# Optimization experiments

Measured on AMD Instinct MI355X. Metric: run time of the kernel, lower is better.

## Reference

```python
import jax, jax.numpy as jnp
import numpy as np

NUM_HEADS = 16


def setup_inputs() -> dict:
    key = jax.random.key(0)
    ks = jax.random.split(key, 6)
    B, T, C = 2, 1024, 2048
    H, D = NUM_HEADS, C // NUM_HEADS
    Tc = 1024  # cached tokens
    return {
        "x": jax.random.normal(ks[0], (B, T, C), dtype=jnp.float32),
        "cache_k": jax.random.normal(ks[1], (B, H, Tc, D), dtype=jnp.float32),
        "cache_v": jax.random.normal(ks[2], (B, H, Tc, D), dtype=jnp.float32),
        "W_qkv": jax.random.normal(ks[3], (C, 3 * C), dtype=jnp.float32) * (C ** -0.5),
        "W_proj": jax.random.normal(ks[4], (C, C), dtype=jnp.float32) * (C ** -0.5),
        "b_proj": jnp.zeros((C,), dtype=jnp.float32),
        "seq_start": Tc,
    }


def reference(x, cache_k, cache_v, W_qkv, W_proj, b_proj, seq_start):
    B, T, C = x.shape
    H = NUM_HEADS
    D = C // H
    scale = D ** -0.5

    qkv = (x @ W_qkv).reshape(B, T, 3, H, D)
    # (B, H, T, D)
    q = jnp.transpose(qkv[:, :, 0], (0, 2, 1, 3))
    k = jnp.transpose(qkv[:, :, 1], (0, 2, 1, 3))
    v = jnp.transpose(qkv[:, :, 2], (0, 2, 1, 3))

    # append to KV cache along time axis
    k = jnp.concatenate([cache_k, k], axis=2)
    v = jnp.concatenate([cache_v, v], axis=2)
    k_len = k.shape[2]

    # causal mask on absolute positions: query_pos >= key_pos
    query_pos = seq_start + jnp.arange(T)
    key_pos = jnp.arange(k_len)
    causal = query_pos[:, None] >= key_pos[None, :]  # (T, k_len)

    attn = jnp.einsum("bhqd,bhkd->bhqk", q * scale, k)
    attn = jnp.where(causal[None, None], attn, -jnp.inf)
    attn = jax.nn.softmax(attn, axis=-1)

    out = jnp.einsum("bhqk,bhkd->bhqd", attn, v)
    out = jnp.transpose(out, (0, 2, 1, 3)).reshape(B, T, C)
    out = out @ W_proj + b_proj
    return out, k, v
```

## Files before the change

### kernel.cpp

```cpp
#include <hip/hip_runtime.h>
#include <hip/hip_bf16.h>

typedef __attribute__((ext_vector_type(8))) short bf16x8;
typedef __attribute__((ext_vector_type(4))) float f32x4;
typedef __attribute__((ext_vector_type(16))) float f32x16;

#define DI __device__ __forceinline__

static constexpr int Bb  = 2;
static constexpr int Tt  = 1024;
static constexpr int Cc  = 2048;
static constexpr int Hh  = 16;
static constexpr int Dd  = 128;
static constexpr int TC  = 1024;
static constexpr int CTX = 2048;
static constexpr float QSCALE = 0.08838834764831845f;

DI unsigned short f2bf(float f){
  unsigned u = __builtin_bit_cast(unsigned, f);
  u += 0x7FFFu + ((u >> 16) & 1u);
  return (unsigned short)(u >> 16);
}
DI float bf2f(unsigned short s){
  return __builtin_bit_cast(float, (unsigned)s << 16);
}
DI unsigned pk2(float a, float b){
  return (unsigned)f2bf(a) | ((unsigned)f2bf(b) << 16);
}
DI bf16x8 mk4(unsigned a, unsigned b, unsigned c, unsigned d){
  union{ unsigned u[4]; bf16x8 v; } x;
  x.u[0]=a; x.u[1]=b; x.u[2]=c; x.u[3]=d; return x.v;
}
DI f32x16 mfma32(bf16x8 a, bf16x8 b, f32x16 c){
  return __builtin_amdgcn_mfma_f32_32x32x16_bf16(a, b, c, 0, 0, 0);
}
#define MFMA16(a,b,c) __builtin_amdgcn_mfma_f32_16x16x32_bf16(a,b,c,0,0,0)
DI void gld16(const void* g, void* l){
  __builtin_amdgcn_global_load_lds(
      (const __attribute__((address_space(1))) unsigned int*)g,
      (__attribute__((address_space(3))) unsigned int*)l, 16, 0, 0);
}
DI unsigned ldsoff(const void* p){
  return (unsigned)(size_t)(const __attribute__((address_space(3))) void*)p;
}
template<int OFF>
DI bf16x8 dsr(unsigned addr){
  bf16x8 v;
  if constexpr (OFF == 0)
    asm volatile("ds_read_b128 %0, %1" : "=v"(v) : "v"(addr));
  else
    asm volatile("ds_read_b128 %0, %1 offset:%2" : "=v"(v) : "v"(addr), "i"(OFF));
  return v;
}
#define BARNC   asm volatile("s_barrier")
#define LGKM0   asm volatile("s_waitcnt lgkmcnt(0)")
#define VMCNT4  asm volatile("s_waitcnt vmcnt(4)")
#define VMCNT3  asm volatile("s_waitcnt vmcnt(3)")
#define VMCNT0  asm volatile("s_waitcnt vmcnt(0)")
#define SBAR    __builtin_amdgcn_sched_barrier(0)

DI void transpose_body(const float* in, unsigned short* out,
                       int C, int ostride, int r0, int c0, int mode,
                       unsigned short (*tile)[33]){
  int tx = threadIdx.x & 31, ty = threadIdx.x >> 5;
#pragma unroll
  for(int i=0;i<4;i++){
    int r = r0 + ty + i*8;
    tile[ty + i*8][tx] = f2bf(in[(size_t)r * C + c0 + tx]);
  }
  __syncthreads();
#pragma unroll
  for(int i=0;i<4;i++){
    int c = c0 + ty + i*8;
    int k = r0 + tx;
    int kp;
    if(mode == 0)
      kp = (k & ~24) | ((((k>>3)&3) ^ ((c>>1)&3)) << 3);
    else
      kp = (k & ~56) | ((((k>>3)&7) ^ (c&7)) << 3);
    out[(size_t)c * ostride + kp] = tile[tx][ty + i*8];
  }
}

__global__ __launch_bounds__(256) void fused_pre_k(
    const float* __restrict__ W_qkv, unsigned short* __restrict__ WqkvT,
    const float4* __restrict__ x4, unsigned short* __restrict__ xbf){
  __shared__ unsigned short tile[32][33];
  int bid = blockIdx.x;
  if(bid < 12288){
    int bx = bid % 192, by = bid / 192;
    transpose_body(W_qkv, WqkvT, 6144, 2048, by*32, bx*32, 0, tile);
  } else {
    int idx = (bid - 12288) * 256 + threadIdx.x;
    int m = idx >> 9;
    int c4 = (idx & 511) * 4;
    float4 v = x4[idx];
    int cp = (c4 & ~24) | ((((c4>>3)&3) ^ ((m>>1)&3)) << 3);
    uint2 p; p.x = pk2(v.x, v.y); p.y = pk2(v.z, v.w);
    *(uint2*)(xbf + (size_t)m * Cc + cp) = p;
  }
}

__global__ __launch_bounds__(256, 4) void gemmA_k(
    const unsigned short* __restrict__ A, const unsigned short* __restrict__ BT,
    unsigned short* __restrict__ q_ws, float* __restrict__ out_k,
    float* __restrict__ out_v, unsigned short* __restrict__ Kws,
    unsigned short* __restrict__ Vt,
    const float4* __restrict__ ck, const float4* __restrict__ cv,
    const float* __restrict__ W_proj, unsigned short* __restrict__ WprojT){
  __shared__ unsigned short Al[2][128*32];
  __shared__ unsigned short Bl[2][128*32];
  int bid = blockIdx.x;
  int tid = threadIdx.x;

  if(bid >= 768){
    if(bid < 4864){
      int idx = (bid - 768) * 256 + tid;
      const int per = TC * Dd / 4;
      int bh = idx / per, r = idx - bh * per;
      int dst = bh * (CTX * Dd / 4) + r;
      float4 kv = ck[idx];
      ((float4*)out_k)[dst] = kv;
      ((float4*)out_v)[dst] = cv[idx];
      int key = r >> 5, dq = (r & 31) * 4;
      int dp = (((dq>>3) ^ (key&7)) << 3) | (dq & 7);
      uint2 p; p.x = pk2(kv.x, kv.y); p.y = pk2(kv.z, kv.w);
      *(uint2*)(Kws + ((size_t)bh * CTX + key) * Dd + dp) = p;
    } else if(bid < 8960){
      int b2 = bid - 4864;
      int bx = b2 & 63, by = b2 >> 6;
      transpose_body(W_proj, WprojT, 2048, 2048, by*32, bx*32, 0,
                     (unsigned short(*)[33])&Al[0][0]);
    } else {
      int zz = bid - 8960;
      int bh = zz >> 7, rem = zz & 127;
      int bx = rem & 3, by = rem >> 2;
      transpose_body((const float*)cv + (size_t)bh*131072,
                     Vt + (size_t)bh*262144, 128, CTX, by*32, bx*32, 1,
                     (unsigned short(*)[33])&Al[0][0]);
    }
    return;
  }

  int lane = tid & 63, w = tid >> 6;
  int lr = lane & 15, lg = lane >> 4;
  constexpr int NWG = 768;
  int swz = (bid & 7) * (NWG/8) + (bid >> 3);
  int m0 = (swz & 15) * 128;
  int n0 = (swz >> 4) * 128;
  int wr = (w >> 1) * 64, wc = (w & 1) * 64;
  int fsw = (lg ^ ((lr >> 1) & 3)) << 3;

  unsigned baseAb = ldsoff(Al) + (unsigned)(((wr + lr)*32 + fsw)*2);
  unsigned baseBb = ldsoff(Bl) + (unsigned)(((wc + lr)*32 + fsw)*2);

  f32x4 acc[4][4];
#pragma unroll
  for(int i=0;i<4;i++)
#pragma unroll
    for(int j=0;j<4;j++) acc[i][j] = (f32x4){0.f,0.f,0.f,0.f};

  auto stage = [&](int buf, int k0){
#pragma unroll
    for(int li=0; li<2; li++){
      int rb = w*32 + li*16;
      gld16(A  + (size_t)(m0 + rb + (lane>>2))*Cc + k0 + (lane&3)*8, &Al[buf][rb*32]);
      gld16(BT + (size_t)(n0 + rb + (lane>>2))*Cc + k0 + (lane&3)*8, &Bl[buf][rb*32]);
    }
  };
  stage(0, 0);
  int buf = 0;
#pragma unroll 1
  for(int k0 = 0; k0 < Cc; k0 += 32){
    SBAR;
    if(k0 + 32 < Cc){
      stage(buf^1, k0 + 32);
      SBAR;
      VMCNT4;
    } else {
      SBAR;
      VMCNT0;
    }
    BARNC;
    unsigned aA = baseAb + (unsigned)buf*8192u;
    unsigned aB = baseBb + (unsigned)buf*8192u;
    bf16x8 af[4], bfr[4];
    af[0]  = dsr<0>(aA);    af[1]  = dsr<1024>(aA);
    af[2]  = dsr<2048>(aA); af[3]  = dsr<3072>(aA);
    bfr[0] = dsr<0>(aB);    bfr[1] = dsr<1024>(aB);
    bfr[2] = dsr<2048>(aB); bfr[3] = dsr<3072>(aB);
    LGKM0;
    SBAR;
    __builtin_amdgcn_s_setprio(1);
#pragma unroll
    for(int mi=0;mi<4;mi++)
#pragma unroll
      for(int ni=0;ni<4;ni++)
        acc[mi][ni] = MFMA16(af[mi], bfr[ni], acc[mi][ni]);
    __builtin_amdgcn_s_setprio(0);
    SBAR;
    BARNC;
    buf ^= 1;
  }

#pragma unroll
  for(int mi=0;mi<4;mi++){
#pragma unroll
    for(int ni=0;ni<4;ni++){
      int n = n0 + wc + ni*16 + lr;
      int seg = n >> 11;
      int h = (n >> 7) & 15, d = n & 127;
#pragma unroll
      for(int r=0;r<4;r++){
        int mrow = m0 + wr + mi*16 + lg*4 + r;
        float v = acc[mi][ni][r];
        int b = mrow >> 10, t = mrow & 1023;
        if(seg == 0){
          q_ws[((size_t)(b*Hh + h)*Tt + t)*Dd + d] = f2bf(v * QSCALE);
        } else if(seg == 1){
          int key = TC + t;
          size_t base = (size_t)(b*Hh + h)*CTX + key;
          out_k[base*Dd + d] = v;
          int dp = (((d>>3) ^ (key&7)) << 3) | (d & 7);
          Kws[base*Dd + dp] = f2bf(v);
        } else {
          int key = TC + t;
          out_v[((size_t)(b*Hh + h)*CTX + key)*Dd + d] = v;
          int kp = (key & ~56) | ((((key>>3)&7) ^ (d&7)) << 3);
          Vt[(size_t)(b*Hh + h)*(Dd*CTX) + (size_t)d*CTX + kp] = f2bf(v);
        }
      }
    }
  }
}

__global__ __launch_bounds__(256, 4) void gemmp_k(
    const unsigned short* __restrict__ A, const unsigned short* __restrict__ BT,
    const float* __restrict__ bias, float* __restrict__ outp){
  __shared__ unsigned short Al[2][64*32];
  __shared__ unsigned short Bl[2][128*32];
  int tid = threadIdx.x, lane = tid & 63, w = tid >> 6;
  int lr = lane & 15, lg = lane >> 4;
  int bid = blockIdx.x;
  int swz = (bid & 7) * 64 + (bid >> 3);
  int m0 = (swz & 31) * 64;
  int n0 = (swz >> 5) * 128;
  int wm2 = (w >> 1) * 32, wn2 = (w & 1) * 64;
  int fsw = (lg ^ ((lr >> 1) & 3)) << 3;

  unsigned baseAb = ldsoff(Al) + (unsigned)(((wm2 + lr)*32 + fsw)*2);
  unsigned baseBb = ldsoff(Bl) + (unsigned)(((wn2 + lr)*32 + fsw)*2);

  f32x4 acc[2][4];
#pragma unroll
  for(int i=0;i<2;i++)
#pragma unroll
    for(int j=0;j<4;j++) acc[i][j] = (f32x4){0.f,0.f,0.f,0.f};

  auto stage = [&](int buf, int k0){
    gld16(A + (size_t)(m0 + w*16 + (lane>>2))*Cc + k0 + (lane&3)*8,
          &Al[buf][w*16*32]);
#pragma unroll
    for(int li=0; li<2; li++){
      int rb = w*32 + li*16;
      gld16(BT + (size_t)(n0 + rb + (lane>>2))*Cc + k0 + (lane&3)*8, &Bl[buf][rb*32]);
    }
  };
  stage(0, 0);
  int buf = 0;
#pragma unroll 1
  for(int k0 = 0; k0 < Cc; k0 += 32){
    SBAR;
    if(k0 + 32 < Cc){
      stage(buf^1, k0 + 32);
      SBAR;
      VMCNT3;
    } else {
      SBAR;
      VMCNT0;
    }
    BARNC;
    unsigned aA = baseAb + (unsigned)buf*4096u;
    unsigned aB = baseBb + (unsigned)buf*8192u;
    bf16x8 af[2], bfr[4];
    af[0]  = dsr<0>(aA);    af[1]  = dsr<1024>(aA);
    bfr[0] = dsr<0>(aB);    bfr[1] = dsr<1024>(aB);
    bfr[2] = dsr<2048>(aB); bfr[3] = dsr<3072>(aB);
    LGKM0;
    SBAR;
    __builtin_amdgcn_s_setprio(1);
#pragma unroll
    for(int mi=0;mi<2;mi++)
#pragma unroll
      for(int ni=0;ni<4;ni++)
        acc[mi][ni] = MFMA16(af[mi], bfr[ni], acc[mi][ni]);
    __builtin_amdgcn_s_setprio(0);
    SBAR;
    BARNC;
    buf ^= 1;
  }

#pragma unroll
  for(int mi=0;mi<2;mi++){
#pragma unroll
    for(int ni=0;ni<4;ni++){
      int n = n0 + wn2 + ni*16 + lr;
#pragma unroll
      for(int r=0;r<4;r++){
        int mrow = m0 + wm2 + mi*16 + lg*4 + r;
        outp[(size_t)mrow * Cc + n] = acc[mi][ni][r] + bias[n];
      }
    }
  }
}

__global__ __launch_bounds__(256, 2) void attn_k(
    const unsigned short* __restrict__ q_ws,
    const unsigned short* __restrict__ Kws,
    const unsigned short* __restrict__ Vt,
    float* __restrict__ O0, unsigned short* __restrict__ O1b,
    float* __restrict__ ml){
  __shared__ unsigned short Kl[2][64*128];
  __shared__ unsigned short Vl[2][128*64];
  int tid = threadIdx.x, lane = tid & 63, w = tid >> 6;
  int l31 = lane & 31, hi = lane >> 5, r7 = l31 & 7;
  int qt = blockIdx.x, split = blockIdx.y, bh = blockIdx.z;
  int q0b = qt * 128, qw0 = q0b + w * 32;
  const unsigned short* Kb = Kws + (size_t)bh * CTX * Dd;
  const unsigned short* Vb = Vt  + (size_t)bh * Dd * CTX;

  const unsigned short* qp = q_ws + ((size_t)bh * Tt + qw0 + l31) * Dd + hi * 8;
  bf16x8 qf[8];
#pragma unroll
  for(int ks=0;ks<8;ks++) qf[ks] = *(const bf16x8*)(qp + ks*16);

  f32x16 o[4];
#pragma unroll
  for(int dt=0;dt<4;dt++)
#pragma unroll
    for(int r=0;r<16;r++) o[dt][r] = 0.f;
  float m = -3e38f, l = 0.f;

  int nts = ((TC + q0b + 128) >> 6) >> 1;

  auto stageK = [&](int buf, int j0){
#pragma unroll
    for(int li=0; li<4; li++){
      gld16(Kb + (size_t)(j0 + w*16 + li*4 + (lane>>4))*Dd + (lane&15)*8,
            &Kl[buf][(w*16 + li*4)*128]);
    }
  };
  auto stageV = [&](int buf, int j0){
#pragma unroll
    for(int li=0; li<4; li++){
      gld16(Vb + (size_t)(w*32 + li*8 + (lane>>3))*CTX + j0 + (lane&7)*8,
            &Vl[buf][(w*32 + li*8)*64]);
    }
  };

  stageK(0, split*64); stageV(0, split*64);
  __syncthreads();
  int buf = 0;
#pragma unroll 1
  for(int t = 0; t < nts; t++){
    int j0 = (2*t + split) * 64;
    if(t + 1 < nts){ stageK(buf^1, j0 + 128); stageV(buf^1, j0 + 128); }

    if(j0 <= TC + qw0 + 31){
      f32x16 s0, s1;
#pragma unroll
      for(int r=0;r<16;r++){ s0[r] = 0.f; s1[r] = 0.f; }
#pragma unroll
      for(int ks=0; ks<8; ks++){
        int ub = ((ks*2 + hi) ^ r7) << 3;
        bf16x8 kf0 = *(const bf16x8*)&Kl[buf][l31*128 + ub];
        bf16x8 kf1 = *(const bf16x8*)&Kl[buf][(32+l31)*128 + ub];
        s0 = mfma32(kf0, qf[ks], s0);
        s1 = mfma32(kf1, qf[ks], s1);
      }
      int qabs = TC + qw0 + l31;
      if(j0 + 63 > TC + qw0){
#pragma unroll
        for(int r=0;r<16;r++){
          int kk = (r&3) + 8*(r>>2) + 4*hi;
          if(j0 + kk > qabs)      s0[r] = -1e30f;
          if(j0 + 32 + kk > qabs) s1[r] = -1e30f;
        }
      }
      float tm = fmaxf(s0[0], s1[0]);
#pragma unroll
      for(int r=1;r<16;r++) tm = fmaxf(tm, fmaxf(s0[r], s1[r]));
      tm = fmaxf(tm, __shfl_xor(tm, 32, 64));
      if(!__all(tm - m <= 8.f)){
        float mn = fmaxf(m, tm);
        float alpha = __expf(m - mn);
        m = mn;
        l *= alpha;
        float ar[16];
#pragma unroll
        for(int r=0;r<16;r++){
          int kk = (r&3) + 8*(r>>2) + 4*hi;
          ar[r] = __shfl(alpha, kk, 64);
        }
#pragma unroll
        for(int dt=0;dt<4;dt++)
#pragma unroll
          for(int r=0;r<16;r++) o[dt][r] *= ar[r];
      }
#pragma unroll
      for(int r=0;r<16;r++){ s0[r] = __expf(s0[r] - m); s1[r] = __expf(s1[r] - m); }
      float ts = 0.f;
#pragma unroll
      for(int r=0;r<16;r++) ts += s0[r] + s1[r];
      ts += __shfl_xor(ts, 32, 64);
      l += ts;
#pragma unroll
      for(int ks16=0; ks16<4; ks16++){
        f32x16 p = (ks16 & 2) ? s1 : s0;
        int fb = (ks16 & 1) * 8;
        unsigned e0 = pk2(p[fb+0], p[fb+1]);
        unsigned e1 = pk2(p[fb+2], p[fb+3]);
        unsigned e2 = pk2(p[fb+4], p[fb+5]);
        unsigned e3 = pk2(p[fb+6], p[fb+7]);
        unsigned x0 = __shfl_xor(e0, 32, 64);
        unsigned x1 = __shfl_xor(e1, 32, 64);
        unsigned x2 = __shfl_xor(e2, 32, 64);
        unsigned x3 = __shfl_xor(e3, 32, 64);
        bf16x8 pa = mk4(hi ? x2 : e0, hi ? x3 : e1, hi ? e2 : x0, hi ? e3 : x1);
        int ub = ((ks16*2 + hi) ^ r7) << 3;
#pragma unroll
        for(int dt=0; dt<4; dt++){
          bf16x8 vf = *(const bf16x8*)&Vl[buf][(dt*32 + l31)*64 + ub];
          o[dt] = mfma32(pa, vf, o[dt]);
        }
      }
    }
    __syncthreads();
    buf ^= 1;
  }

  if(split == 0){
#pragma unroll
    for(int dt=0; dt<4; dt++)
#pragma unroll
      for(int r=0; r<16; r++){
        int q = qw0 + (r&3) + 8*(r>>2) + 4*hi;
        O0[((size_t)bh*Tt + q)*Dd + dt*32 + l31] = o[dt][r];
      }
  } else {
#pragma unroll
    for(int dt=0; dt<4; dt++)
#pragma unroll
      for(int r=0; r<16; r++){
        int q = qw0 + (r&3) + 8*(r>>2) + 4*hi;
        O1b[((size_t)bh*Tt + q)*Dd + dt*32 + l31] = f2bf(o[dt][r]);
      }
  }
  if(lane < 32){
    float* mlp = ml + (((size_t)split*32 + bh)*Tt + qw0 + l31)*2;
    mlp[0] = m; mlp[1] = l;
  }
}

__global__ __launch_bounds__(256) void combine_k(
    const float* __restrict__ O0, const unsigned short* __restrict__ O1b,
    const float* __restrict__ ml, unsigned short* __restrict__ attn_ws){
  int tid = threadIdx.x;
  int d = tid & 127, rl = tid >> 7;
  int row = blockIdx.x * 2 + rl;
  int bh = row >> 10, t = row & 1023;
  const float* p0 = ml + ((size_t)bh * Tt + t) * 2;
  const float* p1 = ml + (((size_t)32 + bh) * Tt + t) * 2;
  float m0 = p0[0], l0 = p0[1], m1 = p1[0], l1 = p1[1];
  float M = fmaxf(m0, m1);
  float e0 = __expf(m0 - M), e1 = __expf(m1 - M);
  float inv = 1.f / (l0*e0 + l1*e1);
  size_t off = (size_t)row * Dd + d;
  float v = (O0[off]*e0 + bf2f(O1b[off])*e1) * inv;
  int b = bh >> 4, h = bh & 15;
  int mrow = b * Tt + t;
  int c = h * Dd + d;
  int cp = (c & ~24) | ((((c>>3)&3) ^ ((mrow>>1)&3)) << 3);
  attn_ws[(size_t)mrow * Cc + cp] = f2bf(v);
}

extern "C" void kernel_launch(void* const* d_in, const int* in_sizes, int n_in,
                              void* d_out, int out_size, void* d_ws, size_t ws_size,
                              hipStream_t stream){
  const float* x       = (const float*)d_in[0];
  const float* cache_k = (const float*)d_in[1];
  const float* cache_v = (const float*)d_in[2];
  const float* W_qkv   = (const float*)d_in[3];
  const float* W_proj  = (const float*)d_in[4];
  const float* b_proj  = (const float*)d_in[5];

  float* out   = (float*)d_out;
  float* out_k = out   + (size_t)Bb*Tt*Cc;
  float* out_v = out_k + (size_t)Bb*Hh*CTX*Dd;
  unsigned short* Vt = (unsigned short*)out;

  if(ws_size < (size_t)67108864) return;
  char* ws = (char*)d_ws;
  unsigned short* WqkvT  = (unsigned short*)(ws);
  float*          O0     = (float*)(ws);
  float*          ml     = (float*)(ws + 16777216);
  unsigned short* WprojT = (unsigned short*)(ws + 25165824);
  unsigned short* Kws    = (unsigned short*)(ws + 33554432);
  unsigned short* attn_ws= (unsigned short*)(ws + 33554432);
  unsigned short* q_ws   = (unsigned short*)(ws + 50331648);
  unsigned short* x_bf   = (unsigned short*)(ws + 58720256);
  unsigned short* O1b    = (unsigned short*)(ws + 58720256);

  fused_pre_k<<<dim3(16384), 256, 0, stream>>>(W_qkv, WqkvT, (const float4*)x, x_bf);
  gemmA_k<<<dim3(13056), 256, 0, stream>>>(x_bf, WqkvT, q_ws, out_k, out_v, Kws, Vt,
                                           (const float4*)cache_k, (const float4*)cache_v,
                                           W_proj, WprojT);
  attn_k<<<dim3(8,2,32), 256, 0, stream>>>(q_ws, Kws, Vt, O0, O1b, ml);
  combine_k<<<dim3(16384), 256, 0, stream>>>(O0, O1b, ml, attn_ws);
  gemmp_k<<<dim3(512), 256, 0, stream>>>(attn_ws, WprojT, b_proj, out);
}
```

Before: 202.0 us.

## Move cache/transpose prep into pre-kernel and double-buffer register fragments in GEMMs

The KV-cache copy, K bf16 packing, W_proj transpose and V transpose blocks move out of the QKV GEMM launch into the preprocessing kernel, so the GEMM launch holds only its 768 tiles and has a smaller launch-bounds occupancy hint. Both GEMM main loops are restructured to unroll by two k-steps, with ping-pong register fragments that read the next LDS tile while MFMAs run on the current one. The aim is better overlap of LDS reads and MFMA work and no heterogeneous work mixed into the GEMM grid. The unrolled loop issues wrapped-around extra prefetches on the last iteration, which costs some wasted loads. Register pressure also rises, and the occupancy hint for gemmA_k drops from 4 to 2.

```diff
diff --git a/kernel.cpp b/kernel.cpp
--- a/kernel.cpp
+++ b/kernel.cpp
@@ -84,13 +84,18 @@
 
 __global__ __launch_bounds__(256) void fused_pre_k(
     const float* __restrict__ W_qkv, unsigned short* __restrict__ WqkvT,
-    const float4* __restrict__ x4, unsigned short* __restrict__ xbf){
+    const float4* __restrict__ x4, unsigned short* __restrict__ xbf,
+    const float4* __restrict__ ck, const float4* __restrict__ cv,
+    float4* __restrict__ ok, float4* __restrict__ ov,
+    unsigned short* __restrict__ Kws,
+    const float* __restrict__ W_proj, unsigned short* __restrict__ WprojT,
+    unsigned short* __restrict__ Vt){
   __shared__ unsigned short tile[32][33];
   int bid = blockIdx.x;
   if(bid < 12288){
     int bx = bid % 192, by = bid / 192;
     transpose_body(W_qkv, WqkvT, 6144, 2048, by*32, bx*32, 0, tile);
-  } else {
+  } else if(bid < 16384){
     int idx = (bid - 12288) * 256 + threadIdx.x;
     int m = idx >> 9;
     int c4 = (idx & 511) * 4;
@@ -98,53 +103,42 @@
     int cp = (c4 & ~24) | ((((c4>>3)&3) ^ ((m>>1)&3)) << 3);
     uint2 p; p.x = pk2(v.x, v.y); p.y = pk2(v.z, v.w);
     *(uint2*)(xbf + (size_t)m * Cc + cp) = p;
-  }
-}
-
-__global__ __launch_bounds__(256, 4) void gemmA_k(
+  } else if(bid < 20480){
+    int idx = (bid - 16384) * 256 + threadIdx.x;
+    const int per = TC * Dd / 4;
+    int bh = idx / per, r = idx - bh * per;
+    int dst = bh * (CTX * Dd / 4) + r;
+    float4 kv = ck[idx];
+    ok[dst] = kv;
+    ov[dst] = cv[idx];
+    int key = r >> 5, dq = (r & 31) * 4;
+    int dp = (((dq>>3) ^ (key&7)) << 3) | (dq & 7);
+    uint2 p; p.x = pk2(kv.x, kv.y); p.y = pk2(kv.z, kv.w);
+    *(uint2*)(Kws + ((size_t)bh * CTX + key) * Dd + dp) = p;
+  } else if(bid < 24576){
+    int b2 = bid - 20480;
+    int bx = b2 & 63, by = b2 >> 6;
+    transpose_body(W_proj, WprojT, 2048, 2048, by*32, bx*32, 0, tile);
+  } else {
+    int zz = bid - 24576;
+    int bh = zz >> 7, rem = zz & 127;
+    int bx = rem & 3, by = rem >> 2;
+    transpose_body((const float*)cv + (size_t)bh*131072,
+                   Vt + (size_t)bh*262144, 128, CTX, by*32, bx*32, 1, tile);
+  }
+}
+
+__global__ __launch_bounds__(256, 2) void gemmA_k(
     const unsigned short* __restrict__ A, const unsigned short* __restrict__ BT,
     unsigned short* __restrict__ q_ws, float* __restrict__ out_k,
     float* __restrict__ out_v, unsigned short* __restrict__ Kws,
-    unsigned short* __restrict__ Vt,
-    const float4* __restrict__ ck, const float4* __restrict__ cv,
-    const float* __restrict__ W_proj, unsigned short* __restrict__ WprojT){
+    unsigned short* __restrict__ Vt){
   __shared__ unsigned short Al[2][128*32];
   __shared__ unsigned short Bl[2][128*32];
-  int bid = blockIdx.x;
-  int tid = threadIdx.x;
-
-  if(bid >= 768){
-    if(bid < 4864){
-      int idx = (bid - 768) * 256 + tid;
-      const int per = TC * Dd / 4;
-      int bh = idx / per, r = idx - bh * per;
-      int dst = bh * (CTX * Dd / 4) + r;
-      float4 kv = ck[idx];
-      ((float4*)out_k)[dst] = kv;
-      ((float4*)out_v)[dst] = cv[idx];
-      int key = r >> 5, dq = (r & 31) * 4;
-      int dp = (((dq>>3) ^ (key&7)) << 3) | (dq & 7);
-      uint2 p; p.x = pk2(kv.x, kv.y); p.y = pk2(kv.z, kv.w);
-      *(uint2*)(Kws + ((size_t)bh * CTX + key) * Dd + dp) = p;
-    } else if(bid < 8960){
-      int b2 = bid - 4864;
-      int bx = b2 & 63, by = b2 >> 6;
-      transpose_body(W_proj, WprojT, 2048, 2048, by*32, bx*32, 0,
-                     (unsigned short(*)[33])&Al[0][0]);
-    } else {
-      int zz = bid - 8960;
-      int bh = zz >> 7, rem = zz & 127;
-      int bx = rem & 3, by = rem >> 2;
-      transpose_body((const float*)cv + (size_t)bh*131072,
-                     Vt + (size_t)bh*262144, 128, CTX, by*32, bx*32, 1,
-                     (unsigned short(*)[33])&Al[0][0]);
-    }
-    return;
-  }
-
-  int lane = tid & 63, w = tid >> 6;
+  int tid = threadIdx.x, lane = tid & 63, w = tid >> 6;
   int lr = lane & 15, lg = lane >> 4;
   constexpr int NWG = 768;
+  int bid = blockIdx.x;
   int swz = (bid & 7) * (NWG/8) + (bid >> 3);
   int m0 = (swz & 15) * 128;
   int n0 = (swz >> 4) * 128;
@@ -160,7 +154,8 @@
 #pragma unroll
     for(int j=0;j<4;j++) acc[i][j] = (f32x4){0.f,0.f,0.f,0.f};
 
-  auto stage = [&](int buf, int k0){
+  auto stage = [&](int buf, int kt){
+    int k0 = kt * 32;
 #pragma unroll
     for(int li=0; li<2; li++){
       int rb = w*32 + li*16;
@@ -168,40 +163,46 @@
       gld16(BT + (size_t)(n0 + rb + (lane>>2))*Cc + k0 + (lane&3)*8, &Bl[buf][rb*32]);
     }
   };
-  stage(0, 0);
-  int buf = 0;
+
+  bf16x8 aP[4], bP[4], aN[4], bN[4];
+#define RDFR(BUF, AA, BB) {                                            \
+    unsigned aA = baseAb + (BUF)*8192u, aB = baseBb + (BUF)*8192u;     \
+    AA[0]=dsr<0>(aA);    AA[1]=dsr<1024>(aA);                          \
+    AA[2]=dsr<2048>(aA); AA[3]=dsr<3072>(aA);                          \
+    BB[0]=dsr<0>(aB);    BB[1]=dsr<1024>(aB);                          \
+    BB[2]=dsr<2048>(aB); BB[3]=dsr<3072>(aB); }
+#define MM16(AA, BB) {                                                 \
+    __builtin_amdgcn_s_setprio(1);                                     \
+    _Pragma("unroll")                                                  \
+    for(int mi=0;mi<4;mi++)                                            \
+      _Pragma("unroll")                                                \
+      for(int ni=0;ni<4;ni++)                                          \
+        acc[mi][ni] = MFMA16(AA[mi], BB[ni], acc[mi][ni]);             \
+    __builtin_amdgcn_s_setprio(0); }
+
+  stage(0, 0); stage(1, 1);
+  SBAR; VMCNT4; BARNC;
+  RDFR(0, aP, bP);
+  SBAR; LGKM0; SBAR; BARNC;
+
 #pragma unroll 1
-  for(int k0 = 0; k0 < Cc; k0 += 32){
+  for(int i=0;i<32;i++){
+    stage(0, (2*i+2)&63);
+    SBAR; VMCNT4; BARNC;
+    RDFR(1, aN, bN);
     SBAR;
-    if(k0 + 32 < Cc){
-      stage(buf^1, k0 + 32);
-      SBAR;
-      VMCNT4;
-    } else {
-      SBAR;
-      VMCNT0;
-    }
-    BARNC;
-    unsigned aA = baseAb + (unsigned)buf*8192u;
-    unsigned aB = baseBb + (unsigned)buf*8192u;
-    bf16x8 af[4], bfr[4];
-    af[0]  = dsr<0>(aA);    af[1]  = dsr<1024>(aA);
-    af[2]  = dsr<2048>(aA); af[3]  = dsr<3072>(aA);
-    bfr[0] = dsr<0>(aB);    bfr[1] = dsr<1024>(aB);
-    bfr[2] = dsr<2048>(aB); bfr[3] = dsr<3072>(aB);
-    LGKM0;
+    MM16(aP, bP);
+    SBAR; LGKM0; SBAR; BARNC;
+    stage(1, (2*i+3)&63);
+    SBAR; VMCNT4; BARNC;
+    RDFR(0, aP, bP);
     SBAR;
-    __builtin_amdgcn_s_setprio(1);
-#pragma unroll
-    for(int mi=0;mi<4;mi++)
-#pragma unroll
-      for(int ni=0;ni<4;ni++)
-        acc[mi][ni] = MFMA16(af[mi], bfr[ni], acc[mi][ni]);
-    __builtin_amdgcn_s_setprio(0);
-    SBAR;
-    BARNC;
-    buf ^= 1;
-  }
+    MM16(aN, bN);
+    SBAR; LGKM0; SBAR; BARNC;
+  }
+#undef RDFR
+#undef MM16
+  VMCNT0;
 
 #pragma unroll
   for(int mi=0;mi<4;mi++){
@@ -257,7 +258,8 @@
 #pragma unroll
     for(int j=0;j<4;j++) acc[i][j] = (f32x4){0.f,0.f,0.f,0.f};
 
-  auto stage = [&](int buf, int k0){
+  auto stage = [&](int buf, int kt){
+    int k0 = kt * 32;
     gld16(A + (size_t)(m0 + w*16 + (lane>>2))*Cc + k0 + (lane&3)*8,
           &Al[buf][w*16*32]);
 #pragma unroll
@@ -266,39 +268,45 @@
       gld16(BT + (size_t)(n0 + rb + (lane>>2))*Cc + k0 + (lane&3)*8, &Bl[buf][rb*32]);
     }
   };
-  stage(0, 0);
-  int buf = 0;
+
+  bf16x8 aP[2], bP[4], aN[2], bN[4];
+#define RDFRP(BUF, AA, BB) {                                           \
+    unsigned aA = baseAb + (BUF)*4096u, aB = baseBb + (BUF)*8192u;     \
+    AA[0]=dsr<0>(aA);    AA[1]=dsr<1024>(aA);                          \
+    BB[0]=dsr<0>(aB);    BB[1]=dsr<1024>(aB);                          \
+    BB[2]=dsr<2048>(aB); BB[3]=dsr<3072>(aB); }
+#define MM8(AA, BB) {                                                  \
+    __builtin_amdgcn_s_setprio(1);                                     \
+    _Pragma("unroll")                                                  \
+    for(int mi=0;mi<2;mi++)                                            \
+      _Pragma("unroll")                                                \
+      for(int ni=0;ni<4;ni++)                                          \
+        acc[mi][ni] = MFMA16(AA[mi], BB[ni], acc[mi][ni]);             \
+    __builtin_amdgcn_s_setprio(0); }
+
+  stage(0, 0); stage(1, 1);
+  SBAR; VMCNT3; BARNC;
+  RDFRP(0, aP, bP);
+  SBAR; LGKM0; SBAR; BARNC;
+
 #pragma unroll 1
-  for(int k0 = 0; k0 < Cc; k0 += 32){
+  for(int i=0;i<32;i++){
+    stage(0, (2*i+2)&63);
+    SBAR; VMCNT3; BARNC;
+    RDFRP(1, aN, bN);
     SBAR;
-    if(k0 + 32 < Cc){
-      stage(buf^1, k0 + 32);
-      SBAR;
-      VMCNT3;
-    } else {
-      SBAR;
-      VMCNT0;
-    }
-    BARNC;
-    unsigned aA = baseAb + (unsigned)buf*4096u;
-    unsigned aB = baseBb + (unsigned)buf*8192u;
-    bf16x8 af[2], bfr[4];
-    af[0]  = dsr<0>(aA);    af[1]  = dsr<1024>(aA);
-    bfr[0] = dsr<0>(aB);    bfr[1] = dsr<1024>(aB);
-    bfr[2] = dsr<2048>(aB); bfr[3] = dsr<3072>(aB);
-    LGKM0;
+    MM8(aP, bP);
+    SBAR; LGKM0; SBAR; BARNC;
+    stage(1, (2*i+3)&63);
+    SBAR; VMCNT3; BARNC;
+    RDFRP(0, aP, bP);
     SBAR;
-    __builtin_amdgcn_s_setprio(1);
-#pragma unroll
-    for(int mi=0;mi<2;mi++)
-#pragma unroll
-      for(int ni=0;ni<4;ni++)
-        acc[mi][ni] = MFMA16(af[mi], bfr[ni], acc[mi][ni]);
-    __builtin_amdgcn_s_setprio(0);
-    SBAR;
-    BARNC;
-    buf ^= 1;
-  }
+    MM8(aN, bN);
+    SBAR; LGKM0; SBAR; BARNC;
+  }
+#undef RDFRP
+#undef MM8
+  VMCNT0;
 
 #pragma unroll
   for(int mi=0;mi<2;mi++){
@@ -511,10 +519,11 @@
   unsigned short* x_bf   = (unsigned short*)(ws + 58720256);
   unsigned short* O1b    = (unsigned short*)(ws + 58720256);
 
-  fused_pre_k<<<dim3(16384), 256, 0, stream>>>(W_qkv, WqkvT, (const float4*)x, x_bf);
-  gemmA_k<<<dim3(13056), 256, 0, stream>>>(x_bf, WqkvT, q_ws, out_k, out_v, Kws, Vt,
-                                           (const float4*)cache_k, (const float4*)cache_v,
-                                           W_proj, WprojT);
+  fused_pre_k<<<dim3(28672), 256, 0, stream>>>(
+      W_qkv, WqkvT, (const float4*)x, x_bf,
+      (const float4*)cache_k, (const float4*)cache_v,
+      (float4*)out_k, (float4*)out_v, Kws, W_proj, WprojT, Vt);
+  gemmA_k<<<dim3(768), 256, 0, stream>>>(x_bf, WqkvT, q_ws, out_k, out_v, Kws, Vt);
   attn_k<<<dim3(8,2,32), 256, 0, stream>>>(q_ws, Kws, Vt, O0, O1b, ml);
   combine_k<<<dim3(16384), 256, 0, stream>>>(O0, O1b, ml, attn_ws);
   gemmp_k<<<dim3(512), 256, 0, stream>>>(attn_ws, WprojT, b_proj, out);
```

Result: slower. 211.9 us (+4.9%).

## Triple-buffer GEMM LDS pipelines and move copy/transpose work into pre-kernel

Applied to the files above, without the earlier changes.

Both bf16 GEMM kernels move from double-buffered to triple-buffered LDS staging. Each iteration issues the load for tile s+2 after a single barrier, so global loads run further ahead of the MFMA work. The cache copy, K packing, W_proj transpose and V transpose leave gemmA_k's extra blocks and become extra block ranges of fused_pre_k. gemmA_k now launches only its 768 GEMM tiles, and its occupancy hint drops to 3 because of the larger LDS footprint. The final two stage calls wrap around to tiles 0 and 1 (loads that are never consumed). Separately, the side work no longer overlaps with the GEMM tiles inside one launch.

```diff
diff --git a/kernel.cpp b/kernel.cpp
--- a/kernel.cpp
+++ b/kernel.cpp
@@ -84,13 +84,18 @@
 
 __global__ __launch_bounds__(256) void fused_pre_k(
     const float* __restrict__ W_qkv, unsigned short* __restrict__ WqkvT,
-    const float4* __restrict__ x4, unsigned short* __restrict__ xbf){
+    const float4* __restrict__ x4, unsigned short* __restrict__ xbf,
+    const float4* __restrict__ ck, const float4* __restrict__ cv,
+    float4* __restrict__ ok, float4* __restrict__ ov,
+    unsigned short* __restrict__ Kws,
+    const float* __restrict__ W_proj, unsigned short* __restrict__ WprojT,
+    unsigned short* __restrict__ Vt){
   __shared__ unsigned short tile[32][33];
   int bid = blockIdx.x;
   if(bid < 12288){
     int bx = bid % 192, by = bid / 192;
     transpose_body(W_qkv, WqkvT, 6144, 2048, by*32, bx*32, 0, tile);
-  } else {
+  } else if(bid < 16384){
     int idx = (bid - 12288) * 256 + threadIdx.x;
     int m = idx >> 9;
     int c4 = (idx & 511) * 4;
@@ -98,53 +103,42 @@
     int cp = (c4 & ~24) | ((((c4>>3)&3) ^ ((m>>1)&3)) << 3);
     uint2 p; p.x = pk2(v.x, v.y); p.y = pk2(v.z, v.w);
     *(uint2*)(xbf + (size_t)m * Cc + cp) = p;
-  }
-}
-
-__global__ __launch_bounds__(256, 4) void gemmA_k(
+  } else if(bid < 20480){
+    int idx = (bid - 16384) * 256 + threadIdx.x;
+    const int per = TC * Dd / 4;
+    int bh = idx / per, r = idx - bh * per;
+    int dst = bh * (CTX * Dd / 4) + r;
+    float4 kv = ck[idx];
+    ok[dst] = kv;
+    ov[dst] = cv[idx];
+    int key = r >> 5, dq = (r & 31) * 4;
+    int dp = (((dq>>3) ^ (key&7)) << 3) | (dq & 7);
+    uint2 p; p.x = pk2(kv.x, kv.y); p.y = pk2(kv.z, kv.w);
+    *(uint2*)(Kws + ((size_t)bh * CTX + key) * Dd + dp) = p;
+  } else if(bid < 24576){
+    int b2 = bid - 20480;
+    int bx = b2 & 63, by = b2 >> 6;
+    transpose_body(W_proj, WprojT, 2048, 2048, by*32, bx*32, 0, tile);
+  } else {
+    int zz = bid - 24576;
+    int bh = zz >> 7, rem = zz & 127;
+    int bx = rem & 3, by = rem >> 2;
+    transpose_body((const float*)cv + (size_t)bh*131072,
+                   Vt + (size_t)bh*262144, 128, CTX, by*32, bx*32, 1, tile);
+  }
+}
+
+__global__ __launch_bounds__(256, 3) void gemmA_k(
     const unsigned short* __restrict__ A, const unsigned short* __restrict__ BT,
     unsigned short* __restrict__ q_ws, float* __restrict__ out_k,
     float* __restrict__ out_v, unsigned short* __restrict__ Kws,
-    unsigned short* __restrict__ Vt,
-    const float4* __restrict__ ck, const float4* __restrict__ cv,
-    const float* __restrict__ W_proj, unsigned short* __restrict__ WprojT){
-  __shared__ unsigned short Al[2][128*32];
-  __shared__ unsigned short Bl[2][128*32];
-  int bid = blockIdx.x;
-  int tid = threadIdx.x;
-
-  if(bid >= 768){
-    if(bid < 4864){
-      int idx = (bid - 768) * 256 + tid;
-      const int per = TC * Dd / 4;
-      int bh = idx / per, r = idx - bh * per;
-      int dst = bh * (CTX * Dd / 4) + r;
-      float4 kv = ck[idx];
-      ((float4*)out_k)[dst] = kv;
-      ((float4*)out_v)[dst] = cv[idx];
-      int key = r >> 5, dq = (r & 31) * 4;
-      int dp = (((dq>>3) ^ (key&7)) << 3) | (dq & 7);
-      uint2 p; p.x = pk2(kv.x, kv.y); p.y = pk2(kv.z, kv.w);
-      *(uint2*)(Kws + ((size_t)bh * CTX + key) * Dd + dp) = p;
-    } else if(bid < 8960){
-      int b2 = bid - 4864;
-      int bx = b2 & 63, by = b2 >> 6;
-      transpose_body(W_proj, WprojT, 2048, 2048, by*32, bx*32, 0,
-                     (unsigned short(*)[33])&Al[0][0]);
-    } else {
-      int zz = bid - 8960;
-      int bh = zz >> 7, rem = zz & 127;
-      int bx = rem & 3, by = rem >> 2;
-      transpose_body((const float*)cv + (size_t)bh*131072,
-                     Vt + (size_t)bh*262144, 128, CTX, by*32, bx*32, 1,
-                     (unsigned short(*)[33])&Al[0][0]);
-    }
-    return;
-  }
-
-  int lane = tid & 63, w = tid >> 6;
+    unsigned short* __restrict__ Vt){
+  __shared__ unsigned short Al[3][128*32];
+  __shared__ unsigned short Bl[3][128*32];
+  int tid = threadIdx.x, lane = tid & 63, w = tid >> 6;
   int lr = lane & 15, lg = lane >> 4;
   constexpr int NWG = 768;
+  int bid = blockIdx.x;
   int swz = (bid & 7) * (NWG/8) + (bid >> 3);
   int m0 = (swz & 15) * 128;
   int n0 = (swz >> 4) * 128;
@@ -160,7 +154,8 @@
 #pragma unroll
     for(int j=0;j<4;j++) acc[i][j] = (f32x4){0.f,0.f,0.f,0.f};
 
-  auto stage = [&](int buf, int k0){
+  auto stage = [&](int buf, int kt){
+    int k0 = kt * 32;
 #pragma unroll
     for(int li=0; li<2; li++){
       int rb = w*32 + li*16;
@@ -168,22 +163,20 @@
       gld16(BT + (size_t)(n0 + rb + (lane>>2))*Cc + k0 + (lane&3)*8, &Bl[buf][rb*32]);
     }
   };
-  stage(0, 0);
-  int buf = 0;
+
+  stage(0, 0); stage(1, 1);
+  int bc = 0;
 #pragma unroll 1
-  for(int k0 = 0; k0 < Cc; k0 += 32){
-    SBAR;
-    if(k0 + 32 < Cc){
-      stage(buf^1, k0 + 32);
-      SBAR;
-      VMCNT4;
-    } else {
-      SBAR;
-      VMCNT0;
-    }
+  for(int s = 0; s < 64; s++){
+    SBAR;
+    VMCNT4;
     BARNC;
-    unsigned aA = baseAb + (unsigned)buf*8192u;
-    unsigned aB = baseBb + (unsigned)buf*8192u;
+    SBAR;
+    int bn2 = bc + 2; if(bn2 >= 3) bn2 -= 3;
+    stage(bn2, (s+2)&63);
+    SBAR;
+    unsigned aA = baseAb + (unsigned)bc*8192u;
+    unsigned aB = baseBb + (unsigned)bc*8192u;
     bf16x8 af[4], bfr[4];
     af[0]  = dsr<0>(aA);    af[1]  = dsr<1024>(aA);
     af[2]  = dsr<2048>(aA); af[3]  = dsr<3072>(aA);
@@ -199,9 +192,9 @@
         acc[mi][ni] = MFMA16(af[mi], bfr[ni], acc[mi][ni]);
     __builtin_amdgcn_s_setprio(0);
     SBAR;
-    BARNC;
-    buf ^= 1;
-  }
+    bc += 1; if(bc >= 3) bc = 0;
+  }
+  VMCNT0;
 
 #pragma unroll
   for(int mi=0;mi<4;mi++){
@@ -237,8 +230,8 @@
 __global__ __launch_bounds__(256, 4) void gemmp_k(
     const unsigned short* __restrict__ A, const unsigned short* __restrict__ BT,
     const float* __restrict__ bias, float* __restrict__ outp){
-  __shared__ unsigned short Al[2][64*32];
-  __shared__ unsigned short Bl[2][128*32];
+  __shared__ unsigned short Al[3][64*32];
+  __shared__ unsigned short Bl[3][128*32];
   int tid = threadIdx.x, lane = tid & 63, w = tid >> 6;
   int lr = lane & 15, lg = lane >> 4;
   int bid = blockIdx.x;
@@ -257,7 +250,8 @@
 #pragma unroll
     for(int j=0;j<4;j++) acc[i][j] = (f32x4){0.f,0.f,0.f,0.f};
 
-  auto stage = [&](int buf, int k0){
+  auto stage = [&](int buf, int kt){
+    int k0 = kt * 32;
     gld16(A + (size_t)(m0 + w*16 + (lane>>2))*Cc + k0 + (lane&3)*8,
           &Al[buf][w*16*32]);
 #pragma unroll
@@ -266,22 +260,20 @@
       gld16(BT + (size_t)(n0 + rb + (lane>>2))*Cc + k0 + (lane&3)*8, &Bl[buf][rb*32]);
     }
   };
-  stage(0, 0);
-  int buf = 0;
+
+  stage(0, 0); stage(1, 1);
+  int bc = 0;
 #pragma unroll 1
-  for(int k0 = 0; k0 < Cc; k0 += 32){
-    SBAR;
-    if(k0 + 32 < Cc){
-      stage(buf^1, k0 + 32);
-      SBAR;
-      VMCNT3;
-    } else {
-      SBAR;
-      VMCNT0;
-    }
+  for(int s = 0; s < 64; s++){
+    SBAR;
+    VMCNT3;
     BARNC;
-    unsigned aA = baseAb + (unsigned)buf*4096u;
-    unsigned aB = baseBb + (unsigned)buf*8192u;
+    SBAR;
+    int bn2 = bc + 2; if(bn2 >= 3) bn2 -= 3;
+    stage(bn2, (s+2)&63);
+    SBAR;
+    unsigned aA = baseAb + (unsigned)bc*4096u;
+    unsigned aB = baseBb + (unsigned)bc*8192u;
     bf16x8 af[2], bfr[4];
     af[0]  = dsr<0>(aA);    af[1]  = dsr<1024>(aA);
     bfr[0] = dsr<0>(aB);    bfr[1] = dsr<1024>(aB);
@@ -296,9 +288,9 @@
         acc[mi][ni] = MFMA16(af[mi], bfr[ni], acc[mi][ni]);
     __builtin_amdgcn_s_setprio(0);
     SBAR;
-    BARNC;
-    buf ^= 1;
-  }
+    bc += 1; if(bc >= 3) bc = 0;
+  }
+  VMCNT0;
 
 #pragma unroll
   for(int mi=0;mi<2;mi++){
@@ -511,10 +503,11 @@
   unsigned short* x_bf   = (unsigned short*)(ws + 58720256);
   unsigned short* O1b    = (unsigned short*)(ws + 58720256);
 
-  fused_pre_k<<<dim3(16384), 256, 0, stream>>>(W_qkv, WqkvT, (const float4*)x, x_bf);
-  gemmA_k<<<dim3(13056), 256, 0, stream>>>(x_bf, WqkvT, q_ws, out_k, out_v, Kws, Vt,
-                                           (const float4*)cache_k, (const float4*)cache_v,
-                                           W_proj, WprojT);
+  fused_pre_k<<<dim3(28672), 256, 0, stream>>>(
+      W_qkv, WqkvT, (const float4*)x, x_bf,
+      (const float4*)cache_k, (const float4*)cache_v,
+      (float4*)out_k, (float4*)out_v, Kws, W_proj, WprojT, Vt);
+  gemmA_k<<<dim3(768), 256, 0, stream>>>(x_bf, WqkvT, q_ws, out_k, out_v, Kws, Vt);
   attn_k<<<dim3(8,2,32), 256, 0, stream>>>(q_ws, Kws, Vt, O0, O1b, ml);
   combine_k<<<dim3(16384), 256, 0, stream>>>(O0, O1b, ml, attn_ws);
   gemmp_k<<<dim3(512), 256, 0, stream>>>(attn_ws, WprojT, b_proj, out);
```

New measurement: 211.2 us. 4.6% more time.

## Move cache/weight prep into pre-kernel and widen transpose to 16-byte stores

Applied to the files above, without the earlier changes.

Moves the KV-cache copy, W_proj transpose and V transpose work out of the QKV GEMM kernel into the preprocessing kernel, so the GEMM launch contains only its 768 compute workgroups. The transpose routine now handles 32x64 tiles and writes each output row segment as a single 16-byte store instead of scattered 2-byte stores, halving the number of transpose blocks. This is meant to cut store transactions and stop the GEMM's LDS-heavy, register-limited configuration from also carrying the bandwidth-bound copy work. The pre-kernel becomes longer and runs serially ahead of the GEMM, so any overlap that came from sharing one launch is lost.

```diff
diff --git a/kernel.cpp b/kernel.cpp
--- a/kernel.cpp
+++ b/kernel.cpp
@@ -61,43 +61,76 @@
 
 DI void transpose_body(const float* in, unsigned short* out,
                        int C, int ostride, int r0, int c0, int mode,
-                       unsigned short (*tile)[33]){
-  int tx = threadIdx.x & 31, ty = threadIdx.x >> 5;
-#pragma unroll
-  for(int i=0;i<4;i++){
-    int r = r0 + ty + i*8;
-    tile[ty + i*8][tx] = f2bf(in[(size_t)r * C + c0 + tx]);
+                       unsigned short (*tile)[40]){
+  int tid = threadIdx.x;
+  int tx = tid & 31, ty = tid >> 5;
+#pragma unroll
+  for(int h=0; h<2; h++){
+#pragma unroll
+    for(int i=0; i<4; i++){
+      int r = r0 + ty + i*8;
+      int c = c0 + h*32 + tx;
+      tile[h*32 + tx][ty + i*8] = f2bf(in[(size_t)r * C + c]);
+    }
   }
   __syncthreads();
-#pragma unroll
-  for(int i=0;i<4;i++){
-    int c = c0 + ty + i*8;
-    int k = r0 + tx;
-    int kp;
-    if(mode == 0)
-      kp = (k & ~24) | ((((k>>3)&3) ^ ((c>>1)&3)) << 3);
-    else
-      kp = (k & ~56) | ((((k>>3)&7) ^ (c&7)) << 3);
-    out[(size_t)c * ostride + kp] = tile[tx][ty + i*8];
-  }
+  int c = tid & 63, u = tid >> 6;
+  int cc = c0 + c;
+  int kpu;
+  if(mode == 0){
+    kpu = r0 + (u ^ ((cc>>1)&3)) * 8;
+  } else {
+    int base = r0 & ~56;
+    int gl = ((r0 >> 3) & 7) + u;
+    kpu = base + (gl ^ (cc & 7)) * 8;
+  }
+  uint4 v = *(const uint4*)&tile[c][u*8];
+  *(uint4*)(out + (size_t)cc * ostride + kpu) = v;
 }
 
 __global__ __launch_bounds__(256) void fused_pre_k(
     const float* __restrict__ W_qkv, unsigned short* __restrict__ WqkvT,
-    const float4* __restrict__ x4, unsigned short* __restrict__ xbf){
-  __shared__ unsigned short tile[32][33];
+    const float4* __restrict__ x4, unsigned short* __restrict__ xbf,
+    const float4* __restrict__ ck, const float4* __restrict__ cv,
+    float4* __restrict__ ok, float4* __restrict__ ov,
+    unsigned short* __restrict__ Kws,
+    const float* __restrict__ W_proj, unsigned short* __restrict__ WprojT,
+    unsigned short* __restrict__ Vt){
+  __shared__ __align__(16) unsigned short tile[64][40];
   int bid = blockIdx.x;
-  if(bid < 12288){
-    int bx = bid % 192, by = bid / 192;
-    transpose_body(W_qkv, WqkvT, 6144, 2048, by*32, bx*32, 0, tile);
-  } else {
-    int idx = (bid - 12288) * 256 + threadIdx.x;
+  if(bid < 6144){
+    int bx = bid % 96, by = bid / 96;
+    transpose_body(W_qkv, WqkvT, 6144, 2048, by*32, bx*64, 0, tile);
+  } else if(bid < 10240){
+    int idx = (bid - 6144) * 256 + threadIdx.x;
     int m = idx >> 9;
     int c4 = (idx & 511) * 4;
     float4 v = x4[idx];
     int cp = (c4 & ~24) | ((((c4>>3)&3) ^ ((m>>1)&3)) << 3);
     uint2 p; p.x = pk2(v.x, v.y); p.y = pk2(v.z, v.w);
     *(uint2*)(xbf + (size_t)m * Cc + cp) = p;
+  } else if(bid < 14336){
+    int idx = (bid - 10240) * 256 + threadIdx.x;
+    const int per = TC * Dd / 4;
+    int bh = idx / per, r = idx - bh * per;
+    int dst = bh * (CTX * Dd / 4) + r;
+    float4 kv = ck[idx];
+    ok[dst] = kv;
+    ov[dst] = cv[idx];
+    int key = r >> 5, dq = (r & 31) * 4;
+    int dp = (((dq>>3) ^ (key&7)) << 3) | (dq & 7);
+    uint2 p; p.x = pk2(kv.x, kv.y); p.y = pk2(kv.z, kv.w);
+    *(uint2*)(Kws + ((size_t)bh * CTX + key) * Dd + dp) = p;
+  } else if(bid < 16384){
+    int b2 = bid - 14336;
+    int bx = b2 & 31, by = b2 >> 5;
+    transpose_body(W_proj, WprojT, 2048, 2048, by*32, bx*64, 0, tile);
+  } else {
+    int zz = bid - 16384;
+    int bh = zz >> 6, rem = zz & 63;
+    int bx = rem & 1, by = rem >> 1;
+    transpose_body((const float*)cv + (size_t)bh*131072,
+                   Vt + (size_t)bh*262144, 128, CTX, by*32, bx*64, 1, tile);
   }
 }
 
@@ -105,46 +138,13 @@
     const unsigned short* __restrict__ A, const unsigned short* __restrict__ BT,
     unsigned short* __restrict__ q_ws, float* __restrict__ out_k,
     float* __restrict__ out_v, unsigned short* __restrict__ Kws,
-    unsigned short* __restrict__ Vt,
-    const float4* __restrict__ ck, const float4* __restrict__ cv,
-    const float* __restrict__ W_proj, unsigned short* __restrict__ WprojT){
+    unsigned short* __restrict__ Vt){
   __shared__ unsigned short Al[2][128*32];
   __shared__ unsigned short Bl[2][128*32];
-  int bid = blockIdx.x;
-  int tid = threadIdx.x;
-
-  if(bid >= 768){
-    if(bid < 4864){
-      int idx = (bid - 768) * 256 + tid;
-      const int per = TC * Dd / 4;
-      int bh = idx / per, r = idx - bh * per;
-      int dst = bh * (CTX * Dd / 4) + r;
-      float4 kv = ck[idx];
-      ((float4*)out_k)[dst] = kv;
-      ((float4*)out_v)[dst] = cv[idx];
-      int key = r >> 5, dq = (r & 31) * 4;
-      int dp = (((dq>>3) ^ (key&7)) << 3) | (dq & 7);
-      uint2 p; p.x = pk2(kv.x, kv.y); p.y = pk2(kv.z, kv.w);
-      *(uint2*)(Kws + ((size_t)bh * CTX + key) * Dd + dp) = p;
-    } else if(bid < 8960){
-      int b2 = bid - 4864;
-      int bx = b2 & 63, by = b2 >> 6;
-      transpose_body(W_proj, WprojT, 2048, 2048, by*32, bx*32, 0,
-                     (unsigned short(*)[33])&Al[0][0]);
-    } else {
-      int zz = bid - 8960;
-      int bh = zz >> 7, rem = zz & 127;
-      int bx = rem & 3, by = rem >> 2;
-      transpose_body((const float*)cv + (size_t)bh*131072,
-                     Vt + (size_t)bh*262144, 128, CTX, by*32, bx*32, 1,
-                     (unsigned short(*)[33])&Al[0][0]);
-    }
-    return;
-  }
-
-  int lane = tid & 63, w = tid >> 6;
+  int tid = threadIdx.x, lane = tid & 63, w = tid >> 6;
   int lr = lane & 15, lg = lane >> 4;
   constexpr int NWG = 768;
+  int bid = blockIdx.x;
   int swz = (bid & 7) * (NWG/8) + (bid >> 3);
   int m0 = (swz & 15) * 128;
   int n0 = (swz >> 4) * 128;
@@ -511,10 +511,11 @@
   unsigned short* x_bf   = (unsigned short*)(ws + 58720256);
   unsigned short* O1b    = (unsigned short*)(ws + 58720256);
 
-  fused_pre_k<<<dim3(16384), 256, 0, stream>>>(W_qkv, WqkvT, (const float4*)x, x_bf);
-  gemmA_k<<<dim3(13056), 256, 0, stream>>>(x_bf, WqkvT, q_ws, out_k, out_v, Kws, Vt,
-                                           (const float4*)cache_k, (const float4*)cache_v,
-                                           W_proj, WprojT);
+  fused_pre_k<<<dim3(18432), 256, 0, stream>>>(
+      W_qkv, WqkvT, (const float4*)x, x_bf,
+      (const float4*)cache_k, (const float4*)cache_v,
+      (float4*)out_k, (float4*)out_v, Kws, W_proj, WprojT, Vt);
+  gemmA_k<<<dim3(768), 256, 0, stream>>>(x_bf, WqkvT, q_ws, out_k, out_v, Kws, Vt);
   attn_k<<<dim3(8,2,32), 256, 0, stream>>>(q_ws, Kws, Vt, O0, O1b, ml);
   combine_k<<<dim3(16384), 256, 0, stream>>>(O0, O1b, ml, attn_ws);
   gemmp_k<<<dim3(512), 256, 0, stream>>>(attn_ws, WprojT, b_proj, out);
```

After: 212.1 us. 5.0% more time.
